# Kernel tuning notes

Measured on AMD Instinct MI355X. Metric: run time of the kernel, lower is better.

Reference implementation:

```python
import jax, jax.numpy as jnp
import numpy as np

EPS = 1e-8

def setup_inputs() -> dict:
    key = jax.random.key(0)
    k1, k2, k3 = jax.random.split(key, 3)
    B, N, C = 4, 2048, 512
    x = jax.random.normal(k1, (B, N, C), dtype=jnp.float32)
    w_qkv = jax.random.normal(k2, (C, 3 * C), dtype=jnp.float32) * (C ** -0.5)
    w_proj = jax.random.normal(k3, (C, C), dtype=jnp.float32) * (C ** -0.5)
    b_proj = jnp.zeros((C,), dtype=jnp.float32)
    alpha = jnp.ones((1,), dtype=jnp.float32)
    beta = jnp.ones((1,), dtype=jnp.float32)
    return {"x": x, "w_qkv": w_qkv, "alpha": alpha, "beta": beta,
            "w_proj": w_proj, "b_proj": b_proj}

def reference(x, w_qkv, alpha, beta, w_proj, b_proj):
    B, N, C = x.shape
    H = 8  # num_heads
    D = C // H  # head_dim = 64
    scale = D ** -0.5
    qkv = (x @ w_qkv).reshape(B, N, 3, H, D)
    q = jnp.transpose(qkv[:, :, 0], (0, 2, 1, 3))  # (B,H,N,D)
    k = jnp.transpose(qkv[:, :, 1], (0, 2, 1, 3))
    v = jnp.transpose(qkv[:, :, 2], (0, 2, 1, 3))
    attn = jnp.einsum('bhnd,bhmd->bhnm', q, k) * scale  # (B,H,N,N)
    # sparse branch: relu^2 sum-normalize
    sp = jnp.square(jax.nn.relu(attn))
    attn_sparse = sp / (sp.sum(axis=-1, keepdims=True) + EPS)
    # dense branch: softmax
    attn_dense = jax.nn.softmax(attn, axis=-1)
    a = jax.nn.sigmoid(alpha)
    b = jax.nn.sigmoid(beta)
    wsum = a + b + EPS
    attn_final = (a / wsum) * attn_sparse + (b / wsum) * attn_dense
    out = jnp.einsum('bhnm,bhmd->bhnd', attn_final, v)  # (B,H,N,D)
    out = jnp.transpose(out, (0, 2, 1, 3)).reshape(B, N, C)
    return out @ w_proj + b_proj
```

## Files before the change

kernel.cpp:

```cpp
#include <hip/hip_runtime.h>

typedef unsigned short u16;
typedef unsigned int   u32;
typedef __attribute__((ext_vector_type(8))) __bf16 bf16x8;
typedef __attribute__((ext_vector_type(4))) float  f32x4;
typedef __attribute__((ext_vector_type(4))) u32    u32x4;

#define AS1q __attribute__((address_space(1)))
#define AS3q __attribute__((address_space(3)))

static __device__ __forceinline__ u16 f2bf(float f) {
    u32 u = __builtin_bit_cast(u32, f);
    u32 r = u + 0x7FFFu + ((u >> 16) & 1u);
    return (u16)(r >> 16);
}

static __device__ __forceinline__ bf16x8 ld16(const u16* p) {
    return __builtin_bit_cast(bf16x8, *(const float4*)(const void*)p);
}

static __device__ __forceinline__ f32x4 mfma16(bf16x8 a, bf16x8 b, f32x4 c) {
    return __builtin_amdgcn_mfma_f32_16x16x32_bf16(a, b, c, 0, 0, 0);
}

static __device__ __forceinline__ void gld16(const u16* g, u16* l) {
    __builtin_amdgcn_global_load_lds((const AS1q u32*)g, (AS3q u32*)l, 16, 0, 0);
}

static __device__ __forceinline__ float exp2_fast(float v) {
    float e;
    asm("v_exp_f32 %0, %1" : "=v"(e) : "v"(v));
    return e;
}

static __device__ __forceinline__ u32 cvtpk(float lo, float hi_) {
    u32 d;
    asm("v_cvt_pk_bf16_f32 %0, %1, %2" : "=v"(d) : "v"(lo), "v"(hi_));
    return d;
}

__global__ __launch_bounds__(256) void k_cast_x(const float* __restrict__ x, u16* __restrict__ xb) {
    int i = blockIdx.x * 256 + threadIdx.x;
    float4 v = ((const float4*)x)[i];
    ushort4 o;
    o.x = f2bf(v.x); o.y = f2bf(v.y); o.z = f2bf(v.z); o.w = f2bf(v.w);
    ((ushort4*)xb)[i] = o;
}

__global__ __launch_bounds__(256) void k_transpose_cast(const float* __restrict__ in, u16* __restrict__ out,
                                                        int K, int Nn) {
    __shared__ float tile[32][33];
    int tx = threadIdx.x & 31, ty = threadIdx.x >> 5;
    int k0 = blockIdx.y * 32, n0 = blockIdx.x * 32;
#pragma unroll
    for (int i = 0; i < 4; ++i)
        tile[ty + i * 8][tx] = in[(k0 + ty + i * 8) * Nn + n0 + tx];
    __syncthreads();
#pragma unroll
    for (int i = 0; i < 4; ++i)
        out[(n0 + ty + i * 8) * K + k0 + tx] = f2bf(tile[tx][ty + i * 8]);
}

static __device__ __forceinline__ void stage128x64(const u16* __restrict__ gbase, int ld,
                                                   u16* lds, int tid) {
    int wid = tid >> 6;
#pragma unroll
    for (int i = 0; i < 4; ++i) {
        int idx = i * 256 + tid;
        int row = idx >> 3, c8 = idx & 7;
        int csw = c8 ^ (row & 7);
        gld16(gbase + row * ld + csw * 8, lds + (i * 256 + wid * 64) * 8);
    }
}

static __device__ __forceinline__ bf16x8 frag(const u16* lds, int row, int col16) {
    return ld16(lds + row * 64 + ((col16 ^ (row & 7)) << 3));
}

__global__ __launch_bounds__(256) void k_gemm_qkv(const u16* __restrict__ xb, const u16* __restrict__ wT,
                                                  u16* __restrict__ Qh, u16* __restrict__ Kh,
                                                  u16* __restrict__ VTh) {
    __shared__ __align__(16) u16 at[128 * 64];
    __shared__ __align__(16) u16 bt[128 * 64];
    int tid = threadIdx.x, lane = tid & 63, wid = tid >> 6;
    int tm = blockIdx.x / 12, tn = blockIdx.x % 12;
    int rb = tm * 128, cb = tn * 128;
    int wr = (wid >> 1) * 64, wc = (wid & 1) * 64;
    int l15 = lane & 15, lhi = lane >> 4;
    f32x4 acc[4][4] = {};
    for (int kk = 0; kk < 512; kk += 64) {
        stage128x64(xb + rb * 512 + kk, 512, at, tid);
        stage128x64(wT + cb * 512 + kk, 512, bt, tid);
        __syncthreads();
        bf16x8 af[4][2], bfr[4][2];
#pragma unroll
        for (int m = 0; m < 4; ++m) {
            int row = wr + m * 16 + l15;
            af[m][0] = frag(at, row, lhi);
            af[m][1] = frag(at, row, 4 + lhi);
        }
#pragma unroll
        for (int n = 0; n < 4; ++n) {
            int row = wc + n * 16 + l15;
            bfr[n][0] = frag(bt, row, lhi);
            bfr[n][1] = frag(bt, row, 4 + lhi);
        }
#pragma unroll
        for (int m = 0; m < 4; ++m)
#pragma unroll
            for (int n = 0; n < 4; ++n) {
                acc[m][n] = mfma16(af[m][0], bfr[n][0], acc[m][n]);
                acc[m][n] = mfma16(af[m][1], bfr[n][1], acc[m][n]);
            }
        __syncthreads();
    }
#pragma unroll
    for (int m = 0; m < 4; ++m)
#pragma unroll
        for (int n = 0; n < 4; ++n)
#pragma unroll
            for (int r = 0; r < 4; ++r) {
                int R  = rb + wr + m * 16 + lhi * 4 + r;
                int Cg = cb + wc + n * 16 + l15;
                int b = R >> 11, nseq = R & 2047;
                int s = Cg >> 9, rm = Cg & 511, h = rm >> 6, d = rm & 63;
                int bh = (b << 3) + h;
                float v = acc[m][n][r];
                if (s == 0)      Qh[(bh * 2048 + nseq) * 64 + d] = f2bf(v * 0.1803368801111244f);
                else if (s == 1) Kh[(bh * 2048 + nseq) * 64 + d] = f2bf(v);
                else             VTh[(bh * 64 + d) * 2048 + nseq] = f2bf(v);
            }
}

#define ATTN_STEP(BUF)                                                           \
    {                                                                            \
        f32x4 s[2][2];                                                           \
        _Pragma("unroll")                                                        \
        for (int kt = 0; kt < 2; ++kt) {                                         \
            int row = kap + 2 * kt;                                              \
            const u16* kbp = &kls[BUF][0] + row * 64;                            \
            bf16x8 kf0 = ld16(kbp + ((lhi ^ (row & 7)) << 3));                   \
            bf16x8 kf1 = ld16(kbp + (((4 + lhi) ^ (row & 7)) << 3));             \
            _Pragma("unroll")                                                    \
            for (int qg = 0; qg < 2; ++qg) {                                     \
                s[qg][kt] = mfma16(kf0, qa[qg][0], z);                           \
                s[qg][kt] = mfma16(kf1, qa[qg][1], s[qg][kt]);                   \
            }                                                                    \
        }                                                                        \
        bf16x8 pfd[2], pfs[2];                                                   \
        _Pragma("unroll")                                                        \
        for (int qg = 0; qg < 2; ++qg) {                                         \
            float ed[2][4], ps[2][4];                                            \
            _Pragma("unroll")                                                    \
            for (int kt = 0; kt < 2; ++kt)                                       \
                _Pragma("unroll")                                                \
                for (int r = 0; r < 4; ++r) {                                    \
                    float v = s[qg][kt][r];                                      \
                    float e = exp2_fast(v);                                      \
                    float t = fmaxf(v, 0.f);                                     \
                    ed[kt][r] = e; ps[kt][r] = t * t;                            \
                }                                                                \
            pfd[qg] = __builtin_bit_cast(bf16x8, (u32x4){                        \
                cvtpk(ed[0][0], ed[0][1]), cvtpk(ed[1][0], ed[1][1]),            \
                cvtpk(ed[0][2], ed[0][3]), cvtpk(ed[1][2], ed[1][3])});          \
            pfs[qg] = __builtin_bit_cast(bf16x8, (u32x4){                        \
                cvtpk(ps[0][0], ps[0][1]), cvtpk(ps[1][0], ps[1][1]),            \
                cvtpk(ps[0][2], ps[0][3]), cvtpk(ps[1][2], ps[1][3])});          \
        }                                                                        \
        _Pragma("unroll")                                                        \
        for (int n = 0; n < 4; ++n) {                                            \
            int row = n * 16 + l15;                                              \
            bf16x8 vf = ld16(&vls[BUF][0] + row * 32 + ((lhi ^ (row & 3)) << 3));\
            _Pragma("unroll")                                                    \
            for (int qg = 0; qg < 2; ++qg) {                                     \
                accd[qg][n] = mfma16(pfd[qg], vf, accd[qg][n]);                  \
                accs[qg][n] = mfma16(pfs[qg], vf, accs[qg][n]);                  \
            }                                                                    \
        }                                                                        \
        _Pragma("unroll")                                                        \
        for (int qg = 0; qg < 2; ++qg) {                                         \
            dend[qg] = mfma16(pfd[qg], onesf, dend[qg]);                         \
            dens[qg] = mfma16(pfs[qg], onesf, dens[qg]);                         \
        }                                                                        \
    }

__global__ __launch_bounds__(256) void k_attn(const u16* __restrict__ Qh, const u16* __restrict__ Kh,
                                              const u16* __restrict__ VTh, const float* __restrict__ alpha,
                                              const float* __restrict__ beta, u16* __restrict__ AO) {
    __shared__ __align__(16) u16 kls[2][32 * 64];
    __shared__ __align__(16) u16 vls[2][64 * 32];
    int tid = threadIdx.x, lane = tid & 63, wid = tid >> 6;
    int l15 = lane & 15, lhi = lane >> 4;
    int wg = (blockIdx.x & 7) * 64 + (blockIdx.x >> 3);
    int bh = wg >> 4;
    int qb = (wg & 15) << 7;
    const u16* Qp = Qh + bh * (2048 * 64);
    const u16* Kp = Kh + bh * (2048 * 64);
    const u16* Vp = VTh + bh * (2048 * 64);
    int qbase = qb + wid * 32;
    bf16x8 qa[2][2];
#pragma unroll
    for (int qg = 0; qg < 2; ++qg) {
        int row = qbase + qg * 16 + l15;
        qa[qg][0] = ld16(Qp + row * 64 + lhi * 8);
        qa[qg][1] = ld16(Qp + row * 64 + 32 + lhi * 8);
    }
    int kap = 8 * (l15 >> 2) + 4 * ((l15 >> 1) & 1) + (l15 & 1);
    f32x4 accd[2][4] = {}, accs[2][4] = {};
    f32x4 dend[2] = {}, dens[2] = {};
    const f32x4 z = {0.f, 0.f, 0.f, 0.f};
    const bf16x8 onesf = __builtin_bit_cast(bf16x8, (u32x4){0x3F803F80u, 0x3F803F80u,
                                                            0x3F803F80u, 0x3F803F80u});

    int krow = tid >> 3, kc8 = tid & 7;
    int vrow = tid >> 2, vc4 = tid & 3;
    const u16* kg = Kp + krow * 64 + ((kc8 ^ (krow & 7)) << 3);
    const u16* vg = Vp + vrow * 2048 + ((vc4 ^ (vrow & 3)) << 3);

    gld16(kg, &kls[0][0] + tid * 8);
    gld16(vg, &vls[0][0] + tid * 8);
    asm volatile("s_waitcnt vmcnt(0)" ::: "memory");
    __builtin_amdgcn_s_barrier();
    const u16* kgp = kg + 32 * 64;
    const u16* vgp = vg + 32;

    for (int kb = 0; kb < 2048; kb += 64) {
        gld16(kgp, &kls[1][0] + tid * 8);
        gld16(vgp, &vls[1][0] + tid * 8);
        kgp += 32 * 64; vgp += 32;
        asm volatile("s_waitcnt vmcnt(2)" ::: "memory");
        __builtin_amdgcn_s_barrier();
        ATTN_STEP(0)
        asm volatile("" ::: "memory");
        __builtin_amdgcn_s_barrier();
        if (kb + 64 < 2048) {
            gld16(kgp, &kls[0][0] + tid * 8);
            gld16(vgp, &vls[0][0] + tid * 8);
            kgp += 32 * 64; vgp += 32;
            asm volatile("s_waitcnt vmcnt(2)" ::: "memory");
        } else {
            asm volatile("s_waitcnt vmcnt(0)" ::: "memory");
        }
        __builtin_amdgcn_s_barrier();
        ATTN_STEP(1)
        asm volatile("" ::: "memory");
        __builtin_amdgcn_s_barrier();
    }
    float sa = 1.f / (1.f + __expf(-alpha[0]));
    float sb = 1.f / (1.f + __expf(-beta[0]));
    float wsum = sa + sb + 1e-8f;
    float wa = sa / wsum, wb = sb / wsum;
    int b = bh >> 3, h = bh & 7;
#pragma unroll
    for (int qg = 0; qg < 2; ++qg) {
        float id[4], isr[4];
#pragma unroll
        for (int r = 0; r < 4; ++r) {
            id[r]  = wb / dend[qg][r];
            isr[r] = wa / (dens[qg][r] + 1e-8f);
        }
#pragma unroll
        for (int n = 0; n < 4; ++n)
#pragma unroll
            for (int r = 0; r < 4; ++r) {
                int R  = b * 2048 + qbase + qg * 16 + lhi * 4 + r;
                int Cg = h * 64 + n * 16 + l15;
                float o = isr[r] * accs[qg][n][r] + id[r] * accd[qg][n][r];
                AO[R * 512 + Cg] = f2bf(o);
            }
    }
}

__global__ __launch_bounds__(256) void k_gemm_proj(const u16* __restrict__ AO, const u16* __restrict__ wT,
                                                   const float* __restrict__ bproj, float* __restrict__ out) {
    __shared__ __align__(16) u16 at[128 * 64];
    __shared__ __align__(16) u16 bt[128 * 64];
    int tid = threadIdx.x, lane = tid & 63, wid = tid >> 6;
    int tm = blockIdx.x >> 2, tn = blockIdx.x & 3;
    int rb = tm * 128, cb = tn * 128;
    int wr = (wid >> 1) * 64, wc = (wid & 1) * 64;
    int l15 = lane & 15, lhi = lane >> 4;
    f32x4 acc[4][4] = {};
    for (int kk = 0; kk < 512; kk += 64) {
        stage128x64(AO + rb * 512 + kk, 512, at, tid);
        stage128x64(wT + cb * 512 + kk, 512, bt, tid);
        __syncthreads();
        bf16x8 af[4][2], bfr[4][2];
#pragma unroll
        for (int m = 0; m < 4; ++m) {
            int row = wr + m * 16 + l15;
            af[m][0] = frag(at, row, lhi);
            af[m][1] = frag(at, row, 4 + lhi);
        }
#pragma unroll
        for (int n = 0; n < 4; ++n) {
            int row = wc + n * 16 + l15;
            bfr[n][0] = frag(bt, row, lhi);
            bfr[n][1] = frag(bt, row, 4 + lhi);
        }
#pragma unroll
        for (int m = 0; m < 4; ++m)
#pragma unroll
            for (int n = 0; n < 4; ++n) {
                acc[m][n] = mfma16(af[m][0], bfr[n][0], acc[m][n]);
                acc[m][n] = mfma16(af[m][1], bfr[n][1], acc[m][n]);
            }
        __syncthreads();
    }
#pragma unroll
    for (int m = 0; m < 4; ++m)
#pragma unroll
        for (int n = 0; n < 4; ++n)
#pragma unroll
            for (int r = 0; r < 4; ++r) {
                int R  = rb + wr + m * 16 + lhi * 4 + r;
                int Cg = cb + wc + n * 16 + l15;
                out[R * 512 + Cg] = acc[m][n][r] + bproj[Cg];
            }
}

extern "C" void kernel_launch(void* const* d_in, const int* in_sizes, int n_in,
                              void* d_out, int out_size, void* d_ws, size_t ws_size,
                              hipStream_t stream) {
    const float* x      = (const float*)d_in[0];
    const float* w_qkv  = (const float*)d_in[1];
    const float* alpha  = (const float*)d_in[2];
    const float* beta   = (const float*)d_in[3];
    const float* w_proj = (const float*)d_in[4];
    const float* b_proj = (const float*)d_in[5];
    float* out = (float*)d_out;
    char* w = (char*)d_ws;
    u16* xb     = (u16*)(w);
    u16* wqkvT  = (u16*)(w + 8388608);
    u16* wprojT = (u16*)(w + 9961472);
    u16* Qh     = (u16*)(w + 10485760);
    u16* Kh     = (u16*)(w + 18874368);
    u16* VTh    = (u16*)(w + 27262976);
    u16* AO     = xb;

    k_cast_x<<<dim3(4096), dim3(256), 0, stream>>>(x, xb);
    k_transpose_cast<<<dim3(48, 16), dim3(256), 0, stream>>>(w_qkv, wqkvT, 512, 1536);
    k_transpose_cast<<<dim3(16, 16), dim3(256), 0, stream>>>(w_proj, wprojT, 512, 512);
    k_gemm_qkv<<<dim3(768), dim3(256), 0, stream>>>(xb, wqkvT, Qh, Kh, VTh);
    k_attn<<<dim3(512), dim3(256), 0, stream>>>(Qh, Kh, VTh, alpha, beta, AO);
    k_gemm_proj<<<dim3(256), dim3(256), 0, stream>>>(AO, wprojT, b_proj, out);
}
```

Baseline: 145.3 us.

## Double-buffer 64-key tiles per stage to halve barrier count in attention loop

The attention main loop now stages 64 keys (K and V^T) per LDS buffer instead of 32, loading two rows per thread and processing each buffer as two 32-key sub-steps. This halves the number of barrier and wait points per key sweep, and keeps a full 64-key prefetch in flight during compute. It doubles LDS use per block (32 KB), which may reduce occupancy, and it changes the V swizzle to an 8-way XOR across 64-wide rows.

New measurement: 145.5 us. About the same (+0.1%).

```diff
diff --git a/kernel.cpp b/kernel.cpp
--- a/kernel.cpp
+++ b/kernel.cpp
@@ -132,12 +132,12 @@
             }
 }
 
-#define ATTN_STEP(BUF)                                                           \
+#define ATTN_SUB(BUF, KS)                                                        \
     {                                                                            \
         f32x4 s[2][2];                                                           \
         _Pragma("unroll")                                                        \
         for (int kt = 0; kt < 2; ++kt) {                                         \
-            int row = kap + 2 * kt;                                              \
+            int row = (KS)*32 + kap + 2 * kt;                                    \
             const u16* kbp = &kls[BUF][0] + row * 64;                            \
             bf16x8 kf0 = ld16(kbp + ((lhi ^ (row & 7)) << 3));                   \
             bf16x8 kf1 = ld16(kbp + (((4 + lhi) ^ (row & 7)) << 3));             \
@@ -170,7 +170,8 @@
         _Pragma("unroll")                                                        \
         for (int n = 0; n < 4; ++n) {                                            \
             int row = n * 16 + l15;                                              \
-            bf16x8 vf = ld16(&vls[BUF][0] + row * 32 + ((lhi ^ (row & 3)) << 3));\
+            bf16x8 vf = ld16(&vls[BUF][0] + row * 64 +                           \
+                             ((((KS)*4 + lhi) ^ (row & 7)) << 3));               \
             _Pragma("unroll")                                                    \
             for (int qg = 0; qg < 2; ++qg) {                                     \
                 accd[qg][n] = mfma16(pfd[qg], vf, accd[qg][n]);                  \
@@ -187,8 +188,8 @@
 __global__ __launch_bounds__(256) void k_attn(const u16* __restrict__ Qh, const u16* __restrict__ Kh,
                                               const u16* __restrict__ VTh, const float* __restrict__ alpha,
                                               const float* __restrict__ beta, u16* __restrict__ AO) {
-    __shared__ __align__(16) u16 kls[2][32 * 64];
-    __shared__ __align__(16) u16 vls[2][64 * 32];
+    __shared__ __align__(16) u16 kls[2][64 * 64];
+    __shared__ __align__(16) u16 vls[2][64 * 64];
     int tid = threadIdx.x, lane = tid & 63, wid = tid >> 6;
     int l15 = lane & 15, lhi = lane >> 4;
     int wg = (blockIdx.x & 7) * 64 + (blockIdx.x >> 3);
@@ -212,37 +213,35 @@
     const bf16x8 onesf = __builtin_bit_cast(bf16x8, (u32x4){0x3F803F80u, 0x3F803F80u,
                                                             0x3F803F80u, 0x3F803F80u});
 
-    int krow = tid >> 3, kc8 = tid & 7;
-    int vrow = tid >> 2, vc4 = tid & 3;
-    const u16* kg = Kp + krow * 64 + ((kc8 ^ (krow & 7)) << 3);
-    const u16* vg = Vp + vrow * 2048 + ((vc4 ^ (vrow & 3)) << 3);
-
-    gld16(kg, &kls[0][0] + tid * 8);
-    gld16(vg, &vls[0][0] + tid * 8);
-    asm volatile("s_waitcnt vmcnt(0)" ::: "memory");
-    __builtin_amdgcn_s_barrier();
-    const u16* kgp = kg + 32 * 64;
-    const u16* vgp = vg + 32;
-
-    for (int kb = 0; kb < 2048; kb += 64) {
-        gld16(kgp, &kls[1][0] + tid * 8);
-        gld16(vgp, &vls[1][0] + tid * 8);
-        kgp += 32 * 64; vgp += 32;
-        asm volatile("s_waitcnt vmcnt(2)" ::: "memory");
-        __builtin_amdgcn_s_barrier();
-        ATTN_STEP(0)
-        asm volatile("" ::: "memory");
-        __builtin_amdgcn_s_barrier();
-        if (kb + 64 < 2048) {
-            gld16(kgp, &kls[0][0] + tid * 8);
-            gld16(vgp, &vls[0][0] + tid * 8);
-            kgp += 32 * 64; vgp += 32;
-            asm volatile("s_waitcnt vmcnt(2)" ::: "memory");
+    int srow = tid >> 3, sc8 = tid & 7;
+    const u16* kg0 = Kp + srow * 64 + ((sc8 ^ (srow & 7)) << 3);
+    const u16* kg1 = Kp + (srow + 32) * 64 + ((sc8 ^ ((srow + 32) & 7)) << 3);
+    const u16* vg0 = Vp + srow * 2048 + ((sc8 ^ (srow & 7)) << 3);
+    const u16* vg1 = Vp + (srow + 32) * 2048 + ((sc8 ^ ((srow + 32) & 7)) << 3);
+
+    gld16(kg0, &kls[0][0] + tid * 8);
+    gld16(kg1, &kls[0][0] + 2048 + tid * 8);
+    gld16(vg0, &vls[0][0] + tid * 8);
+    gld16(vg1, &vls[0][0] + 2048 + tid * 8);
+    int koff = 64 * 64, voff = 64;
+
+    for (int g = 0; g < 32; ++g) {
+        int cur = g & 1;
+        if (g + 1 < 32) {
+            u16* kd = &kls[cur ^ 1][0];
+            u16* vd = &vls[cur ^ 1][0];
+            gld16(kg0 + koff, kd + tid * 8);
+            gld16(kg1 + koff, kd + 2048 + tid * 8);
+            gld16(vg0 + voff, vd + tid * 8);
+            gld16(vg1 + voff, vd + 2048 + tid * 8);
+            koff += 64 * 64; voff += 64;
+            asm volatile("s_waitcnt vmcnt(4)" ::: "memory");
         } else {
             asm volatile("s_waitcnt vmcnt(0)" ::: "memory");
         }
         __builtin_amdgcn_s_barrier();
-        ATTN_STEP(1)
+        ATTN_SUB(cur, 0)
+        ATTN_SUB(cur, 1)
         asm volatile("" ::: "memory");
         __builtin_amdgcn_s_barrier();
     }
```
